# Kernel optimization log

Measured on AMD Instinct MI355X. Metric: run time of the kernel, lower is better.

The kernel has to match this reference:

```python
import jax, jax.numpy as jnp
import numpy as np
from jax import lax

B, C, H, W = 8, 128, 256, 256
OUT_CH = 64
IN_CH = C * 9  # 1152: module's in_channels = 9 * image channels (unfold with 3x3 kernel)


def setup_inputs() -> dict:
    key = jax.random.key(0)
    k1, k2, k3 = jax.random.split(key, 3)
    x = jax.random.normal(k1, (B, C, H, W), dtype=jnp.float32)
    style = jax.random.normal(k2, (B, IN_CH), dtype=jnp.float32)
    # learned parameter: torch.randn(out_channels, in_channels, 1, 1) -> store as (out, in)
    weight = jax.random.normal(k3, (OUT_CH, IN_CH), dtype=jnp.float32)
    return {"x": x, "style": style, "weight": weight}


def reference(x, style, weight):
    b, c, h, w = x.shape
    out_ch, in_ch = weight.shape  # in_ch == c * 9
    # unfold column ordering is (c, kh, kw), so the flattened weight is exactly a
    # 3x3 conv kernel: (out, c*9) -> (out, c, 3, 3)
    w33 = weight.reshape(out_ch, c, 3, 3)
    # style.view(B,1,in_ch,1,1) * weight -> per-sample modulated 3x3 kernels
    w_mod = style.reshape(b, 1, c, 3, 3) * w33[None]  # (B, out, c, 3, 3)

    def conv_one(xi, wi):
        # xi: (c, h, w), wi: (out, c, 3, 3); SAME padding matches padding=(1,1)
        return lax.conv_general_dilated(
            xi[None], wi, window_strides=(1, 1), padding="SAME",
            dimension_numbers=("NCHW", "OIHW", "NCHW"))[0]

    out = jax.vmap(conv_one)(x, w_mod)  # (B, out, h, w)
    return out
```

## Files before the change

kernel.cpp:

```cpp
#include <hip/hip_runtime.h>
#include <hip/hip_bf16.h>

#define BATCH 8
#define CIN   128
#define HH    256
#define WW    256
#define OUTC  64
#define INCH  1152
#define HW    (HH*WW)

typedef __attribute__((ext_vector_type(8))) short short8;
typedef __attribute__((ext_vector_type(4))) float f32x4;

__device__ __forceinline__ unsigned short bf16r(float f) {
    unsigned u = __builtin_bit_cast(unsigned, f);
    u += 0x7fffu + ((u >> 16) & 1u);
    return (unsigned short)(u >> 16);
}

__global__ void __launch_bounds__(256) wmod_kernel(const float* __restrict__ weight,
                                                   const float* __restrict__ style,
                                                   unsigned short* __restrict__ wmod) {
    int i = blockIdx.x * 256 + threadIdx.x;
    if (i >= BATCH * 9 * OUTC * CIN) return;
    int c    = i & (CIN - 1);
    int rest = i >> 7;
    int o    = rest & (OUTC - 1);
    int bt   = rest >> 6;
    int tap  = bt % 9;
    int b    = bt / 9;
    int k    = c * 9 + tap;
    float v = weight[o * INCH + k] * style[b * INCH + k];
    wmod[i] = bf16r(v);
}

template <bool GW>
__global__ void __launch_bounds__(256, 3) conv_kernel(
    const float* __restrict__ x,
    const unsigned short* __restrict__ wmod,
    const float* __restrict__ weight,
    const float* __restrict__ style,
    float* __restrict__ out)
{
    __shared__ __align__(16) unsigned short xs_sm[340 * 72];

    const int tid = threadIdx.x;
    const int bx  = blockIdx.x;
    const int b   = blockIdx.y;
    const int h0  = (bx >> 3) * 8;
    const int w0  = (bx & 7) * 32;

    const int wv  = tid >> 6;
    const int l15 = tid & 15;
    const int kg  = (tid >> 4) & 3;

    int prow[4], pcol[4];
#pragma unroll
    for (int ni = 0; ni < 4; ++ni) {
        int p = wv * 64 + ni * 16 + l15;
        prow[ni] = p >> 5;
        pcol[ni] = p & 31;
    }

    f32x4 acc[4][4];
#pragma unroll
    for (int mi = 0; mi < 4; ++mi)
#pragma unroll
        for (int ni = 0; ni < 4; ++ni) acc[mi][ni] = (f32x4){0.f, 0.f, 0.f, 0.f};

    for (int chunk = 0; chunk < 2; ++chunk) {
        __syncthreads();

        const float* xb = x + ((size_t)(b * CIN + chunk * 64)) * HW;
        for (int t = tid; t < 2720; t += 256) {
            int cg  = t / 340;
            int s   = t - cg * 340;
            int r   = s / 34;
            int col = s - r * 34;
            int h = h0 - 1 + r, w = w0 - 1 + col;
            bool ok = ((unsigned)h < HH) && ((unsigned)w < WW);
            int off = h * WW + w;
            const float* xc = xb + (size_t)(cg * 8) * HW;
            short8 sv;
#pragma unroll
            for (int j = 0; j < 8; ++j) {
                float f = ok ? xc[(size_t)j * HW + off] : 0.f;
                sv[j] = (short)bf16r(f);
            }
            *(short8*)&xs_sm[s * 72 + cg * 8] = sv;
        }
        __syncthreads();

        const unsigned short* wmb = wmod + ((size_t)(b * 9) * OUTC) * CIN + chunk * 64;
#pragma unroll
        for (int tap = 0; tap < 9; ++tap) {
            const int kh = tap / 3, kw = tap % 3;

            short8 A[4][2];
            if (GW) {
                const unsigned short* wt = wmb + (size_t)tap * OUTC * CIN;
#pragma unroll
                for (int mi = 0; mi < 4; ++mi)
#pragma unroll
                    for (int kt = 0; kt < 2; ++kt)
                        A[mi][kt] = *(const short8*)(wt + (mi * 16 + l15) * CIN +
                                                     kt * 32 + kg * 8);
            } else {
#pragma unroll
                for (int mi = 0; mi < 4; ++mi)
#pragma unroll
                    for (int kt = 0; kt < 2; ++kt) {
                        int o = mi * 16 + l15;
#pragma unroll
                        for (int j = 0; j < 8; ++j) {
                            int c = chunk * 64 + kt * 32 + kg * 8 + j;
                            int k = c * 9 + tap;
                            A[mi][kt][j] = (short)bf16r(weight[o * INCH + k] *
                                                        style[b * INCH + k]);
                        }
                    }
            }

            int bb[4];
#pragma unroll
            for (int ni = 0; ni < 4; ++ni)
                bb[ni] = ((prow[ni] + kh) * 34 + pcol[ni] + kw) * 72 + kg * 8;

#pragma unroll
            for (int kt = 0; kt < 2; ++kt) {
                short8 Bv[4];
#pragma unroll
                for (int ni = 0; ni < 4; ++ni)
                    Bv[ni] = *(const short8*)&xs_sm[bb[ni] + kt * 32];
#pragma unroll
                for (int mi = 0; mi < 4; ++mi)
#pragma unroll
                    for (int ni = 0; ni < 4; ++ni)
                        acc[mi][ni] = __builtin_amdgcn_mfma_f32_16x16x32_bf16(
                            A[mi][kt], Bv[ni], acc[mi][ni], 0, 0, 0);
            }
        }
    }

    float* op = out + ((size_t)b * OUTC) * HW;
#pragma unroll
    for (int mi = 0; mi < 4; ++mi) {
#pragma unroll
        for (int ni = 0; ni < 4; ++ni) {
            int p = wv * 64 + ni * 16 + l15;
            int h = h0 + (p >> 5), w = w0 + (p & 31);
#pragma unroll
            for (int r = 0; r < 4; ++r) {
                int o = mi * 16 + kg * 4 + r;
                op[(size_t)o * HW + h * WW + w] = acc[mi][ni][r];
            }
        }
    }
}

extern "C" void kernel_launch(void* const* d_in, const int* in_sizes, int n_in,
                              void* d_out, int out_size, void* d_ws, size_t ws_size,
                              hipStream_t stream) {
    const float* x      = (const float*)d_in[0];
    const float* style  = (const float*)d_in[1];
    const float* weight = (const float*)d_in[2];
    float* out = (float*)d_out;

    const size_t wmod_bytes = (size_t)BATCH * 9 * OUTC * CIN * sizeof(unsigned short);
    if (ws_size >= wmod_bytes) {
        int total = BATCH * 9 * OUTC * CIN;
        wmod_kernel<<<(total + 255) / 256, 256, 0, stream>>>(weight, style,
                                                             (unsigned short*)d_ws);
        conv_kernel<true><<<dim3(256, BATCH), 256, 0, stream>>>(
            x, (const unsigned short*)d_ws, nullptr, nullptr, out);
    } else {
        conv_kernel<false><<<dim3(256, BATCH), 256, 0, stream>>>(
            x, nullptr, weight, style, out);
    }
}
```

Measured before the change: 262.0 us.

## Halve LDS tile with 32-channel chunks and XOR-swizzled layout for higher occupancy

Splits the input-channel reduction into four 32-channel chunks instead of two 64-channel chunks. This shrinks the shared-memory input tile from 340x72 to 170x64 shorts, and the launch bound is raised to 4 waves-per-EU occupancy. The padded row layout is replaced by an XOR swizzle that packs two pixels per 64-element row, meant to avoid LDS bank conflicts without padding. In exchange there are twice as many chunk barriers and halo reloads per block, and fewer registers are available per thread.

```diff
diff --git a/kernel.cpp b/kernel.cpp
--- a/kernel.cpp
+++ b/kernel.cpp
@@ -35,14 +35,14 @@
 }
 
 template <bool GW>
-__global__ void __launch_bounds__(256, 3) conv_kernel(
+__global__ void __launch_bounds__(256, 4) conv_kernel(
     const float* __restrict__ x,
     const unsigned short* __restrict__ wmod,
     const float* __restrict__ weight,
     const float* __restrict__ style,
     float* __restrict__ out)
 {
-    __shared__ __align__(16) unsigned short xs_sm[340 * 72];
+    __shared__ __align__(16) unsigned short xs_sm[170 * 64];
 
     const int tid = threadIdx.x;
     const int bx  = blockIdx.x;
@@ -68,11 +68,11 @@
 #pragma unroll
         for (int ni = 0; ni < 4; ++ni) acc[mi][ni] = (f32x4){0.f, 0.f, 0.f, 0.f};
 
-    for (int chunk = 0; chunk < 2; ++chunk) {
-        __syncthreads();
+    for (int chunk = 0; chunk < 4; ++chunk) {
+        if (chunk) __syncthreads();
 
-        const float* xb = x + ((size_t)(b * CIN + chunk * 64)) * HW;
-        for (int t = tid; t < 2720; t += 256) {
+        const float* xb = x + ((size_t)(b * CIN + chunk * 32)) * HW;
+        for (int t = tid; t < 1360; t += 256) {
             int cg  = t / 340;
             int s   = t - cg * 340;
             int r   = s / 34;
@@ -87,58 +87,51 @@
                 float f = ok ? xc[(size_t)j * HW + off] : 0.f;
                 sv[j] = (short)bf16r(f);
             }
-            *(short8*)&xs_sm[s * 72 + cg * 8] = sv;
+            int q = s >> 1;
+            int g = (((s & 1) << 2) | cg) ^ (q & 7);
+            *(short8*)&xs_sm[q * 64 + g * 8] = sv;
         }
         __syncthreads();
 
-        const unsigned short* wmb = wmod + ((size_t)(b * 9) * OUTC) * CIN + chunk * 64;
+        const unsigned short* wmb = wmod + ((size_t)(b * 9) * OUTC) * CIN + chunk * 32;
 #pragma unroll
         for (int tap = 0; tap < 9; ++tap) {
             const int kh = tap / 3, kw = tap % 3;
 
-            short8 A[4][2];
+            short8 A[4];
             if (GW) {
                 const unsigned short* wt = wmb + (size_t)tap * OUTC * CIN;
 #pragma unroll
                 for (int mi = 0; mi < 4; ++mi)
-#pragma unroll
-                    for (int kt = 0; kt < 2; ++kt)
-                        A[mi][kt] = *(const short8*)(wt + (mi * 16 + l15) * CIN +
-                                                     kt * 32 + kg * 8);
+                    A[mi] = *(const short8*)(wt + (mi * 16 + l15) * CIN + kg * 8);
             } else {
 #pragma unroll
-                for (int mi = 0; mi < 4; ++mi)
+                for (int mi = 0; mi < 4; ++mi) {
+                    int o = mi * 16 + l15;
 #pragma unroll
-                    for (int kt = 0; kt < 2; ++kt) {
-                        int o = mi * 16 + l15;
-#pragma unroll
-                        for (int j = 0; j < 8; ++j) {
-                            int c = chunk * 64 + kt * 32 + kg * 8 + j;
-                            int k = c * 9 + tap;
-                            A[mi][kt][j] = (short)bf16r(weight[o * INCH + k] *
-                                                        style[b * INCH + k]);
-                        }
+                    for (int j = 0; j < 8; ++j) {
+                        int c = chunk * 32 + kg * 8 + j;
+                        int k = c * 9 + tap;
+                        A[mi][j] = (short)bf16r(weight[o * INCH + k] *
+                                                style[b * INCH + k]);
                     }
+                }
             }
 
-            int bb[4];
+            short8 Bv[4];
 #pragma unroll
-            for (int ni = 0; ni < 4; ++ni)
-                bb[ni] = ((prow[ni] + kh) * 34 + pcol[ni] + kw) * 72 + kg * 8;
-
+            for (int ni = 0; ni < 4; ++ni) {
+                int s = (prow[ni] + kh) * 34 + pcol[ni] + kw;
+                int q = s >> 1;
+                int g = (((s & 1) << 2) | kg) ^ (q & 7);
+                Bv[ni] = *(const short8*)&xs_sm[q * 64 + g * 8];
+            }
 #pragma unroll
-            for (int kt = 0; kt < 2; ++kt) {
-                short8 Bv[4];
+            for (int mi = 0; mi < 4; ++mi)
 #pragma unroll
                 for (int ni = 0; ni < 4; ++ni)
-                    Bv[ni] = *(const short8*)&xs_sm[bb[ni] + kt * 32];
-#pragma unroll
-                for (int mi = 0; mi < 4; ++mi)
-#pragma unroll
-                    for (int ni = 0; ni < 4; ++ni)
-                        acc[mi][ni] = __builtin_amdgcn_mfma_f32_16x16x32_bf16(
-                            A[mi][kt], Bv[ni], acc[mi][ni], 0, 0, 0);
-            }
+                    acc[mi][ni] = __builtin_amdgcn_mfma_f32_16x16x32_bf16(
+                        A[mi], Bv[ni], acc[mi][ni], 0, 0, 0);
         }
     }
 
```

After: 248.7 us. 5.1% less time.
